# Performance work log

Hardware: AMD Instinct MI355X
Metric: run time of the kernel (lower is better)

## Reference

```python
import jax, jax.numpy as jnp
import numpy as np

EPS = 1e-5

def _layer_norm(x, w, b):
    mu = jnp.mean(x, axis=-1, keepdims=True)
    var = jnp.mean(jnp.square(x - mu), axis=-1, keepdims=True)
    return (x - mu) * jax.lax.rsqrt(var + EPS) * w + b

def setup_inputs() -> dict:
    key = jax.random.key(0)
    ks = jax.random.split(key, 8)
    B, S, D = 8, 2048, 1024
    image_features = jax.random.normal(ks[0], (B, S, D), dtype=jnp.float32)
    text_features = jax.random.normal(ks[1], (B, S, D), dtype=jnp.float32)
    ln_w = jnp.ones((D,), dtype=jnp.float32)
    ln_b = jnp.zeros((D,), dtype=jnp.float32)
    lim = 1.0 / np.sqrt(D)
    W_img = jax.random.uniform(ks[2], (D, D), minval=-lim, maxval=lim, dtype=jnp.float32)
    b_img = jax.random.uniform(ks[3], (D,), minval=-lim, maxval=lim, dtype=jnp.float32)
    W_txt = jax.random.uniform(ks[4], (D, D), minval=-lim, maxval=lim, dtype=jnp.float32)
    b_txt = jax.random.uniform(ks[5], (D,), minval=-lim, maxval=lim, dtype=jnp.float32)
    return {"image_features": image_features, "text_features": text_features,
            "ln_w": ln_w, "ln_b": ln_b, "W_img": W_img, "b_img": b_img,
            "W_txt": W_txt, "b_txt": b_txt}

def reference(image_features, text_features, ln_w, ln_b, W_img, b_img, W_txt, b_txt):
    D = image_features.shape[-1]
    scale = D ** (-0.5)
    image_norm = _layer_norm(image_features, ln_w, ln_b)
    text_norm = _layer_norm(text_features, ln_w, ln_b)
    # torch Linear: x @ W^T + b
    image_proj = jnp.einsum('bsd,ed->bse', image_norm, W_img) + b_img  # [B,Si,D]
    text_proj = jnp.einsum('btd,ed->bte', text_norm, W_txt) + b_txt    # [B,St,D]
    attn = jnp.einsum('bsd,btd->bst', image_proj, text_proj) * scale   # [B,Si,St]
    attn = jax.nn.softmax(attn, axis=-1)
    image_out = jnp.einsum('bst,btd->bsd', attn, text_proj)            # [B,Si,D]
    text_out = jnp.einsum('bst,bsd->btd', attn, image_proj)            # [B,St,D]
    return (image_out, text_out)
```

## Files before the change

### kernel.cpp

```cpp
#include <hip/hip_runtime.h>


#define DEV __device__ __forceinline__

typedef short s16x8 __attribute__((ext_vector_type(8)));
typedef float f32x4 __attribute__((ext_vector_type(4)));

DEV unsigned short f2bf(float f){
  unsigned u = __float_as_uint(f);
  u = (u + 0x7fffu + ((u >> 16) & 1u)) >> 16;
  return (unsigned short)u;
}
DEV float bf2f(unsigned short s){ return __uint_as_float(((unsigned)s) << 16); }

DEV void ldsload16(const void* g, void* l){
  __builtin_amdgcn_global_load_lds((const __attribute__((address_space(1))) void*)g,
                                   (__attribute__((address_space(3))) void*)l, 16, 0, 0);
}

__global__ __launch_bounds__(256) void k_cvt(const float* __restrict__ src,
                                             unsigned short* __restrict__ dst, int n4){
  int i = blockIdx.x * 256 + threadIdx.x;
  if (i < n4){
    float4 v = ((const float4*)src)[i];
    ushort4 o;
    o.x = f2bf(v.x); o.y = f2bf(v.y); o.z = f2bf(v.z); o.w = f2bf(v.w);
    ((ushort4*)dst)[i] = o;
  }
}

__global__ __launch_bounds__(256) void k_ln(const float* __restrict__ x,
                                            const float* __restrict__ w,
                                            const float* __restrict__ b,
                                            unsigned short* __restrict__ y){
  int row = blockIdx.x, tid = threadIdx.x;
  float4 v = ((const float4*)(x + (size_t)row * 1024))[tid];
  float s  = v.x + v.y + v.z + v.w;
  float s2 = v.x*v.x + v.y*v.y + v.z*v.z + v.w*v.w;
  #pragma unroll
  for (int o = 32; o > 0; o >>= 1){ s += __shfl_xor(s, o, 64); s2 += __shfl_xor(s2, o, 64); }
  __shared__ float sh[8];
  int wv = tid >> 6, ln = tid & 63;
  if (!ln){ sh[wv] = s; sh[4 + wv] = s2; }
  __syncthreads();
  s  = sh[0] + sh[1] + sh[2] + sh[3];
  s2 = sh[4] + sh[5] + sh[6] + sh[7];
  float mean = s * (1.f/1024.f);
  float var  = s2 * (1.f/1024.f) - mean * mean;
  float rstd = rsqrtf(var + 1e-5f);
  float4 w4 = ((const float4*)w)[tid];
  float4 b4 = ((const float4*)b)[tid];
  ushort4 o;
  o.x = f2bf((v.x-mean)*rstd*w4.x + b4.x);
  o.y = f2bf((v.y-mean)*rstd*w4.y + b4.y);
  o.z = f2bf((v.z-mean)*rstd*w4.z + b4.z);
  o.w = f2bf((v.w-mean)*rstd*w4.w + b4.w);
  ((ushort4*)(y + (size_t)row * 1024))[tid] = o;
}

#define STG(MAT, BASE, LD, T, H) do{                                              \
  ldsload16((BASE) + (size_t)(wave*16 + sfr) * (LD) + (T)*64 + (H)*32 + sq*8,     \
            &MAT[(T)&1][H][wave][0]);                                             \
  ldsload16((BASE) + (size_t)(wave*16 + 128 + sfr) * (LD) + (T)*64 + (H)*32 + sq*8,\
            &MAT[(T)&1][H][wave + 8][0]);                                         \
}while(0)

template<int OUT_BF16>
__global__ __launch_bounds__(512, 2) void k_gemm256(const unsigned short* __restrict__ A,
                                                    const unsigned short* __restrict__ Bt,
                                                    void* __restrict__ C,
                                                    const float* __restrict__ bias, float scale,
                                                    int K, int lda, int ldb, int ldc,
                                                    long sA, long sB, long sC,
                                                    int NBX, int NBY){
  __shared__ __align__(16) unsigned short As[2][2][16][512];
  __shared__ __align__(16) unsigned short Bs[2][2][16][512];
  int nwg = gridDim.x;
  int bid = blockIdx.x;
  int swz = (bid & 7) * (nwg >> 3) + (bid >> 3);
  int bx = swz % NBX; int rem = swz / NBX;
  int by = rem % NBY; int bz = rem / NBY;

  int tid = threadIdx.x, lane = tid & 63, wave = tid >> 6;
  int wm = wave >> 2, wn = wave & 3;
  int q = lane >> 4, fr = lane & 15;
  const unsigned short* Ab = A  + (size_t)bz * sA + (size_t)by * 256 * lda;
  const unsigned short* Bb = Bt + (size_t)bz * sB + (size_t)bx * 256 * ldb;
  int v   = (lane & 7) ^ ((lane >> 3) & 7);
  int sfr = 2 * (lane >> 3) + (v >> 2);
  int sq  = v & 3;
  int roff = ((fr >> 1) << 6) + (((q + ((fr & 1) << 2)) ^ ((fr >> 1) & 7)) << 3);
  int NT = K >> 6;

  f32x4 acc[8][4];
  #pragma unroll
  for (int m = 0; m < 8; ++m)
    #pragma unroll
    for (int n = 0; n < 4; ++n) acc[m][n] = f32x4{0.f, 0.f, 0.f, 0.f};

  STG(As, Ab, lda, 0, 0); STG(Bs, Bb, ldb, 0, 0);
  STG(As, Ab, lda, 0, 1); STG(Bs, Bb, ldb, 0, 1);
  STG(As, Ab, lda, 1, 0); STG(Bs, Bb, ldb, 1, 0);
  asm volatile("s_waitcnt vmcnt(8)");
  __builtin_amdgcn_s_barrier();

  for (int t = 0; t < NT; ++t){
    const int buf = t & 1;
    s16x8 bfr[4];
    #pragma unroll
    for (int ph = 0; ph < 4; ++ph){
      const int kk = ph >> 1;
      const unsigned short* Ah = &As[buf][kk][0][0];
      const unsigned short* Bh = &Bs[buf][kk][0][0];
      s16x8 af[4];
      if ((ph & 1) == 0){
        #pragma unroll
        for (int n = 0; n < 4; ++n)  bfr[n] = *(const s16x8*)&Bh[(wn*4 + n)*512 + roff];
        #pragma unroll
        for (int mi = 0; mi < 4; ++mi) af[mi] = *(const s16x8*)&Ah[(wm*8 + mi)*512 + roff];
      } else {
        #pragma unroll
        for (int mi = 0; mi < 4; ++mi) af[mi] = *(const s16x8*)&Ah[(wm*8 + 4 + mi)*512 + roff];
      }
      if (ph == 0){ if (t + 1 < NT) STG(As, Ab, lda, t + 1, 1); }
      if (ph == 1){ if (t + 1 < NT) STG(Bs, Bb, ldb, t + 1, 1); }
      if (ph == 2){ if (t + 2 < NT) STG(As, Ab, lda, t + 2, 0); }
      if (ph == 3){ if (t + 2 < NT) STG(Bs, Bb, ldb, t + 2, 0); }
      __builtin_amdgcn_s_barrier();
      asm volatile("s_waitcnt lgkmcnt(0)");
      __builtin_amdgcn_sched_barrier(0);
      __builtin_amdgcn_s_setprio(1);
      #pragma unroll
      for (int mi = 0; mi < 4; ++mi)
        #pragma unroll
        for (int n = 0; n < 4; ++n)
          acc[(ph&1)*4 + mi][n] = __builtin_amdgcn_mfma_f32_16x16x32_bf16(
              af[mi], bfr[n], acc[(ph&1)*4 + mi][n], 0, 0, 0);
      __builtin_amdgcn_s_setprio(0);
      __builtin_amdgcn_sched_barrier(0);
      if (ph & 1){
        if (t + 2 < NT) asm volatile("s_waitcnt vmcnt(8)");
        else            asm volatile("s_waitcnt vmcnt(0)");
      }
      __builtin_amdgcn_s_barrier();
    }
  }
  size_t cb = (size_t)bz * sC;
  int row0 = by*256 + wm*128 + q*4;
  int col0 = bx*256 + wn*64 + fr;
  #pragma unroll
  for (int m = 0; m < 8; ++m){
    #pragma unroll
    for (int n = 0; n < 4; ++n){
      int col = col0 + n*16;
      float bv = bias ? bias[col] : 0.f;
      #pragma unroll
      for (int j = 0; j < 4; ++j){
        int row = row0 + m*16 + j;
        float vv = acc[m][n][j] * scale + bv;
        if (OUT_BF16) ((unsigned short*)C)[cb + (size_t)row*ldc + col] = f2bf(vv);
        else          ((float*)C)[cb + (size_t)row*ldc + col] = vv;
      }
    }
  }
}

__global__ __launch_bounds__(256) void k_transpose(const unsigned short* __restrict__ src,
                                                   unsigned short* __restrict__ dst,
                                                   int R, int C, long sS, long sD){
  __shared__ __align__(16) unsigned short tile[64 * 64];
  int tid = threadIdx.x;
  const unsigned short* sb = src + (size_t)blockIdx.z * sS;
  unsigned short* db = dst + (size_t)blockIdx.z * sD;
  int r0 = blockIdx.y * 64, c0 = blockIdx.x * 64;
  #pragma unroll
  for (int i = 0; i < 2; ++i){
    int ci = i * 256 + tid;
    int row = ci >> 3, cch = ci & 7;
    int pos = cch ^ (row & 7) ^ (row >> 3);
    uint4 v = *(const uint4*)&sb[(size_t)(r0 + row) * C + c0 + cch * 8];
    *(uint4*)&tile[row * 64 + pos * 8] = v;
  }
  __syncthreads();
  int ocp = tid >> 3, og = tid & 7;
  int oc = ocp * 2;
  union { uint4 v; unsigned short us[8]; } o0, o1;
  #pragma unroll
  for (int k = 0; k < 8; ++k){
    int r = og * 8 + k;
    int pos = (oc >> 3) ^ (r & 7) ^ (r >> 3);
    unsigned pr = *(const unsigned*)&tile[r * 64 + pos * 8 + (oc & 7)];
    o0.us[k] = (unsigned short)(pr & 0xffffu);
    o1.us[k] = (unsigned short)(pr >> 16);
  }
  *(uint4*)&db[(size_t)(c0 + oc    ) * R + r0 + og * 8] = o0.v;
  *(uint4*)&db[(size_t)(c0 + oc + 1) * R + r0 + og * 8] = o1.v;
}

__global__ __launch_bounds__(256) void k_softmax(unsigned short* __restrict__ a){
  size_t row = blockIdx.x;
  unsigned short* p = a + row * 2048;
  int tid = threadIdx.x;
  union { uint4 v; unsigned short us[8]; } in, out;
  in.v = *(const uint4*)&p[tid * 8];
  float x[8];
  #pragma unroll
  for (int j = 0; j < 8; ++j) x[j] = bf2f(in.us[j]);
  float mx = x[0];
  #pragma unroll
  for (int j = 1; j < 8; ++j) mx = fmaxf(mx, x[j]);
  #pragma unroll
  for (int o = 32; o > 0; o >>= 1) mx = fmaxf(mx, __shfl_xor(mx, o, 64));
  __shared__ float sh[8];
  int wv = tid >> 6, ln = tid & 63;
  if (!ln) sh[wv] = mx;
  __syncthreads();
  mx = fmaxf(fmaxf(sh[0], sh[1]), fmaxf(sh[2], sh[3]));
  float sm = 0.f, e[8];
  #pragma unroll
  for (int j = 0; j < 8; ++j){ e[j] = __expf(x[j] - mx); sm += e[j]; }
  #pragma unroll
  for (int o = 32; o > 0; o >>= 1) sm += __shfl_xor(sm, o, 64);
  if (!ln) sh[4 + wv] = sm;
  __syncthreads();
  sm = sh[4] + sh[5] + sh[6] + sh[7];
  float inv = 1.f / sm;
  #pragma unroll
  for (int j = 0; j < 8; ++j) out.us[j] = f2bf(e[j] * inv);
  *(uint4*)&p[tid * 8] = out.v;
}

extern "C" void kernel_launch(void* const* d_in, const int* in_sizes, int n_in,
                              void* d_out, int out_size, void* d_ws, size_t ws_size,
                              hipStream_t stream) {
  const float* img  = (const float*)d_in[0];
  const float* txt  = (const float*)d_in[1];
  const float* lnw  = (const float*)d_in[2];
  const float* lnb  = (const float*)d_in[3];
  const float* Wimg = (const float*)d_in[4];
  const float* bimg = (const float*)d_in[5];
  const float* Wtxt = (const float*)d_in[6];
  const float* btxt = (const float*)d_in[7];
  float* out = (float*)d_out;

  char* ws = (char*)d_ws;
  unsigned short* R1 = (unsigned short*)ws;
  unsigned short* R2 = (unsigned short*)(ws + 67108864);
  unsigned short* WB = (unsigned short*)(ws + 134217728);
  unsigned short* R4 = (unsigned short*)(ws + 138412032);

  const long PB = 2097152;
  const long AB = 4194304;

  k_cvt<<<1024, 256, 0, stream>>>(Wimg, WB,           262144);
  k_cvt<<<1024, 256, 0, stream>>>(Wtxt, WB + 1048576, 262144);
  k_ln<<<16384, 256, 0, stream>>>(img, lnw, lnb, R1);
  k_ln<<<16384, 256, 0, stream>>>(txt, lnw, lnb, R1 + 16777216);
  k_gemm256<1><<<256, 512, 0, stream>>>(R1,            WB,           R2,            bimg, 1.f,
                                        1024, 1024, 1024, 1024, 0, 0, 0, 4, 64);
  k_gemm256<1><<<256, 512, 0, stream>>>(R1 + 16777216, WB + 1048576, R2 + 16777216, btxt, 1.f,
                                        1024, 1024, 1024, 1024, 0, 0, 0, 4, 64);
  dim3 gt(16, 32, 8);
  k_transpose<<<gt, 256, 0, stream>>>(R2,            R1,            2048, 1024, PB, PB);
  k_transpose<<<gt, 256, 0, stream>>>(R2 + 16777216, R1 + 16777216, 2048, 1024, PB, PB);
  k_gemm256<1><<<512, 512, 0, stream>>>(R2, R2 + 16777216, R4, nullptr, 0.03125f,
                                        1024, 1024, 1024, 2048, PB, PB, AB, 8, 8);
  k_softmax<<<16384, 256, 0, stream>>>(R4);
  dim3 gat(32, 32, 8);
  k_transpose<<<gat, 256, 0, stream>>>(R4, R2, 2048, 2048, AB, AB);
  k_gemm256<0><<<256, 512, 0, stream>>>(R4, R1 + 16777216, out, nullptr, 1.f,
                                        2048, 2048, 2048, 1024, AB, PB, PB, 4, 8);
  k_gemm256<0><<<256, 512, 0, stream>>>(R2, R1, out + 16777216, nullptr, 1.f,
                                        2048, 2048, 2048, 1024, AB, PB, PB, 4, 8);
}
```

Baseline: 422.1 us.

## Switch to 128x128 GEMM tiles and fuse softmax with transpose

Replaces the 256x256 eight-wave GEMM, which had a deep multi-phase prefetch pipeline, with a simpler 128x128 four-wave kernel that double-buffers 32-wide K steps. All GEMM launches get four times as many workgroups. The separate softmax and attention transpose kernels are merged into one kernel where each block handles 64 rows, making three passes over each row and transposing through LDS. The trade-off is less data reuse per tile and a less overlapped pipeline. The fused softmax runs only 256 blocks and rereads every row, which may hurt occupancy and bandwidth use.

```diff
diff --git a/kernel.cpp b/kernel.cpp
--- a/kernel.cpp
+++ b/kernel.cpp
@@ -58,23 +58,23 @@
   ((ushort4*)(y + (size_t)row * 1024))[tid] = o;
 }
 
-#define STG(MAT, BASE, LD, T, H) do{                                              \
-  ldsload16((BASE) + (size_t)(wave*16 + sfr) * (LD) + (T)*64 + (H)*32 + sq*8,     \
-            &MAT[(T)&1][H][wave][0]);                                             \
-  ldsload16((BASE) + (size_t)(wave*16 + 128 + sfr) * (LD) + (T)*64 + (H)*32 + sq*8,\
-            &MAT[(T)&1][H][wave + 8][0]);                                         \
+#define STG(MAT, BASE, LD, T) do{                                                 \
+  ldsload16((BASE) + (size_t)(wave*16 + sfr) * (LD) + (T)*32 + sq*8,              \
+            &MAT[(T)&1][wave][0]);                                                \
+  ldsload16((BASE) + (size_t)(wave*16 + 64 + sfr) * (LD) + (T)*32 + sq*8,         \
+            &MAT[(T)&1][wave + 4][0]);                                            \
 }while(0)
 
 template<int OUT_BF16>
-__global__ __launch_bounds__(512, 2) void k_gemm256(const unsigned short* __restrict__ A,
+__global__ __launch_bounds__(256, 3) void k_gemm128(const unsigned short* __restrict__ A,
                                                     const unsigned short* __restrict__ Bt,
                                                     void* __restrict__ C,
                                                     const float* __restrict__ bias, float scale,
                                                     int K, int lda, int ldb, int ldc,
                                                     long sA, long sB, long sC,
                                                     int NBX, int NBY){
-  __shared__ __align__(16) unsigned short As[2][2][16][512];
-  __shared__ __align__(16) unsigned short Bs[2][2][16][512];
+  __shared__ __align__(16) unsigned short As[2][8][512];
+  __shared__ __align__(16) unsigned short Bs[2][8][512];
   int nwg = gridDim.x;
   int bid = blockIdx.x;
   int swz = (bid & 7) * (nwg >> 3) + (bid >> 3);
@@ -82,74 +82,52 @@
   int by = rem % NBY; int bz = rem / NBY;
 
   int tid = threadIdx.x, lane = tid & 63, wave = tid >> 6;
-  int wm = wave >> 2, wn = wave & 3;
+  int wm = wave >> 1, wn = wave & 1;
   int q = lane >> 4, fr = lane & 15;
-  const unsigned short* Ab = A  + (size_t)bz * sA + (size_t)by * 256 * lda;
-  const unsigned short* Bb = Bt + (size_t)bz * sB + (size_t)bx * 256 * ldb;
+  const unsigned short* Ab = A  + (size_t)bz * sA + (size_t)by * 128 * lda;
+  const unsigned short* Bb = Bt + (size_t)bz * sB + (size_t)bx * 128 * ldb;
   int v   = (lane & 7) ^ ((lane >> 3) & 7);
   int sfr = 2 * (lane >> 3) + (v >> 2);
   int sq  = v & 3;
   int roff = ((fr >> 1) << 6) + (((q + ((fr & 1) << 2)) ^ ((fr >> 1) & 7)) << 3);
-  int NT = K >> 6;
-
-  f32x4 acc[8][4];
-  #pragma unroll
-  for (int m = 0; m < 8; ++m)
+  const int NT = K >> 5;
+
+  f32x4 acc[4][4];
+  #pragma unroll
+  for (int m = 0; m < 4; ++m)
     #pragma unroll
     for (int n = 0; n < 4; ++n) acc[m][n] = f32x4{0.f, 0.f, 0.f, 0.f};
 
-  STG(As, Ab, lda, 0, 0); STG(Bs, Bb, ldb, 0, 0);
-  STG(As, Ab, lda, 0, 1); STG(Bs, Bb, ldb, 0, 1);
-  STG(As, Ab, lda, 1, 0); STG(Bs, Bb, ldb, 1, 0);
-  asm volatile("s_waitcnt vmcnt(8)");
+  STG(As, Ab, lda, 0); STG(Bs, Bb, ldb, 0);
+  asm volatile("s_waitcnt vmcnt(0)");
   __builtin_amdgcn_s_barrier();
 
   for (int t = 0; t < NT; ++t){
     const int buf = t & 1;
-    s16x8 bfr[4];
-    #pragma unroll
-    for (int ph = 0; ph < 4; ++ph){
-      const int kk = ph >> 1;
-      const unsigned short* Ah = &As[buf][kk][0][0];
-      const unsigned short* Bh = &Bs[buf][kk][0][0];
-      s16x8 af[4];
-      if ((ph & 1) == 0){
-        #pragma unroll
-        for (int n = 0; n < 4; ++n)  bfr[n] = *(const s16x8*)&Bh[(wn*4 + n)*512 + roff];
-        #pragma unroll
-        for (int mi = 0; mi < 4; ++mi) af[mi] = *(const s16x8*)&Ah[(wm*8 + mi)*512 + roff];
-      } else {
-        #pragma unroll
-        for (int mi = 0; mi < 4; ++mi) af[mi] = *(const s16x8*)&Ah[(wm*8 + 4 + mi)*512 + roff];
-      }
-      if (ph == 0){ if (t + 1 < NT) STG(As, Ab, lda, t + 1, 1); }
-      if (ph == 1){ if (t + 1 < NT) STG(Bs, Bb, ldb, t + 1, 1); }
-      if (ph == 2){ if (t + 2 < NT) STG(As, Ab, lda, t + 2, 0); }
-      if (ph == 3){ if (t + 2 < NT) STG(Bs, Bb, ldb, t + 2, 0); }
-      __builtin_amdgcn_s_barrier();
-      asm volatile("s_waitcnt lgkmcnt(0)");
-      __builtin_amdgcn_sched_barrier(0);
-      __builtin_amdgcn_s_setprio(1);
+    if (t + 1 < NT){ STG(As, Ab, lda, t + 1); STG(Bs, Bb, ldb, t + 1); }
+    s16x8 af[4], bfr[4];
+    #pragma unroll
+    for (int mi = 0; mi < 4; ++mi) af[mi] = *(const s16x8*)&As[buf][wm*4 + mi][roff];
+    #pragma unroll
+    for (int n = 0; n < 4; ++n)   bfr[n]  = *(const s16x8*)&Bs[buf][wn*4 + n][roff];
+    asm volatile("s_waitcnt lgkmcnt(0)");
+    __builtin_amdgcn_sched_barrier(0);
+    __builtin_amdgcn_s_setprio(1);
+    #pragma unroll
+    for (int mi = 0; mi < 4; ++mi)
       #pragma unroll
-      for (int mi = 0; mi < 4; ++mi)
-        #pragma unroll
-        for (int n = 0; n < 4; ++n)
-          acc[(ph&1)*4 + mi][n] = __builtin_amdgcn_mfma_f32_16x16x32_bf16(
-              af[mi], bfr[n], acc[(ph&1)*4 + mi][n], 0, 0, 0);
-      __builtin_amdgcn_s_setprio(0);
-      __builtin_amdgcn_sched_barrier(0);
-      if (ph & 1){
-        if (t + 2 < NT) asm volatile("s_waitcnt vmcnt(8)");
-        else            asm volatile("s_waitcnt vmcnt(0)");
-      }
-      __builtin_amdgcn_s_barrier();
-    }
+      for (int n = 0; n < 4; ++n)
+        acc[mi][n] = __builtin_amdgcn_mfma_f32_16x16x32_bf16(af[mi], bfr[n], acc[mi][n], 0, 0, 0);
+    __builtin_amdgcn_s_setprio(0);
+    __builtin_amdgcn_sched_barrier(0);
+    asm volatile("s_waitcnt vmcnt(0)");
+    __builtin_amdgcn_s_barrier();
   }
   size_t cb = (size_t)bz * sC;
-  int row0 = by*256 + wm*128 + q*4;
-  int col0 = bx*256 + wn*64 + fr;
-  #pragma unroll
-  for (int m = 0; m < 8; ++m){
+  int row0 = by*128 + wm*64 + q*4;
+  int col0 = bx*128 + wn*64 + fr;
+  #pragma unroll
+  for (int m = 0; m < 4; ++m){
     #pragma unroll
     for (int n = 0; n < 4; ++n){
       int col = col0 + n*16;
@@ -197,37 +175,62 @@
   *(uint4*)&db[(size_t)(c0 + oc + 1) * R + r0 + og * 8] = o1.v;
 }
 
-__global__ __launch_bounds__(256) void k_softmax(unsigned short* __restrict__ a){
-  size_t row = blockIdx.x;
-  unsigned short* p = a + row * 2048;
+__global__ __launch_bounds__(256) void k_softmax_t(unsigned short* __restrict__ a,
+                                                   unsigned short* __restrict__ at){
+  __shared__ __align__(16) unsigned short tile[64 * 64];
   int tid = threadIdx.x;
-  union { uint4 v; unsigned short us[8]; } in, out;
-  in.v = *(const uint4*)&p[tid * 8];
-  float x[8];
-  #pragma unroll
-  for (int j = 0; j < 8; ++j) x[j] = bf2f(in.us[j]);
-  float mx = x[0];
-  #pragma unroll
-  for (int j = 1; j < 8; ++j) mx = fmaxf(mx, x[j]);
-  #pragma unroll
-  for (int o = 32; o > 0; o >>= 1) mx = fmaxf(mx, __shfl_xor(mx, o, 64));
-  __shared__ float sh[8];
-  int wv = tid >> 6, ln = tid & 63;
-  if (!ln) sh[wv] = mx;
-  __syncthreads();
-  mx = fmaxf(fmaxf(sh[0], sh[1]), fmaxf(sh[2], sh[3]));
-  float sm = 0.f, e[8];
-  #pragma unroll
-  for (int j = 0; j < 8; ++j){ e[j] = __expf(x[j] - mx); sm += e[j]; }
-  #pragma unroll
-  for (int o = 32; o > 0; o >>= 1) sm += __shfl_xor(sm, o, 64);
-  if (!ln) sh[4 + wv] = sm;
-  __syncthreads();
-  sm = sh[4] + sh[5] + sh[6] + sh[7];
-  float inv = 1.f / sm;
-  #pragma unroll
-  for (int j = 0; j < 8; ++j) out.us[j] = f2bf(e[j] * inv);
-  *(uint4*)&p[tid * 8] = out.v;
+  int r = tid >> 2, sub = tid & 3;
+  size_t boff = (size_t)blockIdx.y * 4194304;
+  int r0 = blockIdx.x * 64;
+  unsigned short* prow = a + boff + (size_t)(r0 + r) * 2048;
+  float mx = -3.0e38f;
+  for (int i = 0; i < 64; ++i){
+    union { uint4 v; unsigned short us[8]; } u;
+    u.v = *(const uint4*)&prow[(sub + 4*i) * 8];
+    #pragma unroll
+    for (int j = 0; j < 8; ++j) mx = fmaxf(mx, bf2f(u.us[j]));
+  }
+  mx = fmaxf(mx, __shfl_xor(mx, 1, 64));
+  mx = fmaxf(mx, __shfl_xor(mx, 2, 64));
+  float s = 0.f;
+  for (int i = 0; i < 64; ++i){
+    union { uint4 v; unsigned short us[8]; } u;
+    u.v = *(const uint4*)&prow[(sub + 4*i) * 8];
+    #pragma unroll
+    for (int j = 0; j < 8; ++j) s += __expf(bf2f(u.us[j]) - mx);
+  }
+  s += __shfl_xor(s, 1, 64);
+  s += __shfl_xor(s, 2, 64);
+  float inv = 1.f / s;
+  int ocp = tid >> 3, og = tid & 7, oc = ocp * 2;
+  for (int cb = 0; cb < 32; ++cb){
+    #pragma unroll
+    for (int jj = 0; jj < 2; ++jj){
+      int j = sub + jj*4;
+      int c8 = cb*8 + j;
+      union { uint4 v; unsigned short us[8]; } u, o;
+      u.v = *(const uint4*)&prow[c8 * 8];
+      #pragma unroll
+      for (int k = 0; k < 8; ++k) o.us[k] = f2bf(__expf(bf2f(u.us[k]) - mx) * inv);
+      *(uint4*)&prow[c8 * 8] = o.v;
+      int pos = j ^ (r & 7) ^ (r >> 3);
+      *(uint4*)&tile[r * 64 + pos * 8] = o.v;
+    }
+    __syncthreads();
+    union { uint4 v; unsigned short us[8]; } o0, o1;
+    #pragma unroll
+    for (int k = 0; k < 8; ++k){
+      int rr = og * 8 + k;
+      int pos = (oc >> 3) ^ (rr & 7) ^ (rr >> 3);
+      unsigned pr = *(const unsigned*)&tile[rr * 64 + pos * 8 + (oc & 7)];
+      o0.us[k] = (unsigned short)(pr & 0xffffu);
+      o1.us[k] = (unsigned short)(pr >> 16);
+    }
+    size_t c0 = (size_t)cb * 64;
+    *(uint4*)&at[boff + (c0 + oc    ) * 2048 + r0 + og * 8] = o0.v;
+    *(uint4*)&at[boff + (c0 + oc + 1) * 2048 + r0 + og * 8] = o1.v;
+    __syncthreads();
+  }
 }
 
 extern "C" void kernel_launch(void* const* d_in, const int* in_sizes, int n_in,
@@ -256,20 +259,19 @@
   k_cvt<<<1024, 256, 0, stream>>>(Wtxt, WB + 1048576, 262144);
   k_ln<<<16384, 256, 0, stream>>>(img, lnw, lnb, R1);
   k_ln<<<16384, 256, 0, stream>>>(txt, lnw, lnb, R1 + 16777216);
-  k_gemm256<1><<<256, 512, 0, stream>>>(R1,            WB,           R2,            bimg, 1.f,
-                                        1024, 1024, 1024, 1024, 0, 0, 0, 4, 64);
-  k_gemm256<1><<<256, 512, 0, stream>>>(R1 + 16777216, WB + 1048576, R2 + 16777216, btxt, 1.f,
-                                        1024, 1024, 1024, 1024, 0, 0, 0, 4, 64);
+  k_gemm128<1><<<1024, 256, 0, stream>>>(R1,            WB,           R2,            bimg, 1.f,
+                                         1024, 1024, 1024, 1024, 0, 0, 0, 8, 128);
+  k_gemm128<1><<<1024, 256, 0, stream>>>(R1 + 16777216, WB + 1048576, R2 + 16777216, btxt, 1.f,
+                                         1024, 1024, 1024, 1024, 0, 0, 0, 8, 128);
   dim3 gt(16, 32, 8);
   k_transpose<<<gt, 256, 0, stream>>>(R2,            R1,            2048, 1024, PB, PB);
   k_transpose<<<gt, 256, 0, stream>>>(R2 + 16777216, R1 + 16777216, 2048, 1024, PB, PB);
-  k_gemm256<1><<<512, 512, 0, stream>>>(R2, R2 + 16777216, R4, nullptr, 0.03125f,
-                                        1024, 1024, 1024, 2048, PB, PB, AB, 8, 8);
-  k_softmax<<<16384, 256, 0, stream>>>(R4);
-  dim3 gat(32, 32, 8);
-  k_transpose<<<gat, 256, 0, stream>>>(R4, R2, 2048, 2048, AB, AB);
-  k_gemm256<0><<<256, 512, 0, stream>>>(R4, R1 + 16777216, out, nullptr, 1.f,
-                                        2048, 2048, 2048, 1024, AB, PB, PB, 4, 8);
-  k_gemm256<0><<<256, 512, 0, stream>>>(R2, R1, out + 16777216, nullptr, 1.f,
-                                        2048, 2048, 2048, 1024, AB, PB, PB, 4, 8);
-}
+  k_gemm128<1><<<2048, 256, 0, stream>>>(R2, R2 + 16777216, R4, nullptr, 0.03125f,
+                                         1024, 1024, 1024, 2048, PB, PB, AB, 16, 16);
+  dim3 gs(32, 8);
+  k_softmax_t<<<gs, 256, 0, stream>>>(R4, R2);
+  k_gemm128<0><<<1024, 256, 0, stream>>>(R4, R1 + 16777216, out, nullptr, 1.f,
+                                         2048, 2048, 2048, 1024, AB, PB, PB, 8, 16);
+  k_gemm128<0><<<1024, 256, 0, stream>>>(R2, R1, out + 16777216, nullptr, 1.f,
+                                         2048, 2048, 2048, 1024, AB, PB, PB, 8, 16);
+}
```

Result: slower. 457.5 us (+8.4%).
